# Kernel optimization log

Hardware: AMD Instinct MI355X
Metric: run time of the kernel (lower is better)

The kernel has to match this reference:

```python
import jax, jax.numpy as jnp
import numpy as np

MODEL = 2048
LATENT = 512
POS = 1024
NH = 16
HD = MODEL // NH        # 128
PHD = POS // NH         # 64
THETA = 50000.0


def _rope_tables(S, dim, base=THETA):
    inv_freq = 1.0 / (base ** (jnp.arange(0, dim, 2, dtype=jnp.float32) / dim))
    t = jnp.arange(S, dtype=jnp.float32)
    freqs = jnp.outer(t, inv_freq)                  # [S, dim/2]
    emb = jnp.concatenate([freqs, freqs], axis=-1)  # [S, dim]
    return jnp.cos(emb), jnp.sin(emb)


def _rotate_half(x):
    h = x.shape[-1] // 2
    return jnp.concatenate([-x[..., h:], x[..., :h]], axis=-1)


def _apply_rope(x, cos, sin):
    # x: [..., S, dim]; cos/sin: [S, dim]
    return x * cos + _rotate_half(x) * sin


def setup_inputs() -> dict:
    key = jax.random.key(0)
    ks = jax.random.split(key, 16)
    std = 0.02
    d = {
        'x':      jax.random.normal(ks[0], (2, 2048, MODEL), jnp.float32),
        'w_qkv':  jax.random.normal(ks[1], (MODEL, 3 * LATENT), jnp.float32) * std,
        'b_qkv':  jnp.zeros((3 * LATENT,), jnp.float32),
        'w_qup':  jax.random.normal(ks[2], (LATENT, MODEL), jnp.float32) * std,
        'b_qup':  jnp.zeros((MODEL,), jnp.float32),
        'w_kup':  jax.random.normal(ks[3], (LATENT, MODEL), jnp.float32) * std,
        'b_kup':  jnp.zeros((MODEL,), jnp.float32),
        'w_vup':  jax.random.normal(ks[4], (LATENT, MODEL), jnp.float32) * std,
        'b_vup':  jnp.zeros((MODEL,), jnp.float32),
        'w_qpos': jax.random.normal(ks[5], (LATENT, POS), jnp.float32) * std,
        'b_qpos': jnp.zeros((POS,), jnp.float32),
        'w_kpos': jax.random.normal(ks[6], (MODEL, PHD), jnp.float32) * std,
        'b_kpos': jnp.zeros((PHD,), jnp.float32),
        'w_o':    jax.random.normal(ks[7], (MODEL, MODEL), jnp.float32) * std,
        'b_o':    jnp.zeros((MODEL,), jnp.float32),
    }
    return d


def reference(x, w_qkv, b_qkv, w_qup, b_qup, w_kup, b_kup, w_vup, b_vup,
              w_qpos, b_qpos, w_kpos, b_kpos, w_o, b_o):
    B, S, _ = x.shape
    # fused down-projection into shared latent
    latent_qkv = x @ w_qkv + b_qkv                       # [B,S,3L]
    lq, lk, lv = jnp.split(latent_qkv, 3, axis=-1)       # each [B,S,L]

    cos, sin = _rope_tables(S, PHD)

    # decoupled positional key (shared across heads), RoPE on sub-slice
    pos_k = x @ w_kpos + b_kpos                          # [B,S,PHD]
    pos_k = _apply_rope(pos_k, cos, sin)

    # up-projections
    q = (lq @ w_qup + b_qup).reshape(B, S, NH, HD).transpose(0, 2, 1, 3)
    k = (lk @ w_kup + b_kup).reshape(B, S, NH, HD).transpose(0, 2, 1, 3)
    v = (lv @ w_vup + b_vup).reshape(B, S, NH, HD).transpose(0, 2, 1, 3)

    pos_q = (lq @ w_qpos + b_qpos).reshape(B, S, NH, PHD).transpose(0, 2, 1, 3)
    pos_q = _apply_rope(pos_q, cos, sin)                 # [B,NH,S,PHD]

    pos_kh = jnp.broadcast_to(pos_k[:, None], (B, NH, S, PHD))
    q = jnp.concatenate([q, pos_q], axis=-1)             # [B,NH,S,HD+PHD]
    k = jnp.concatenate([k, pos_kh], axis=-1)

    scale = 1.0 / jnp.sqrt(jnp.asarray(HD + PHD, x.dtype))
    scores = jnp.einsum('bhqd,bhkd->bhqk', q, k) * scale
    causal = jnp.tril(jnp.ones((S, S), bool))
    scores = jnp.where(causal, scores, jnp.finfo(scores.dtype).min)
    p = jax.nn.softmax(scores, axis=-1)
    attn = jnp.einsum('bhqk,bhkd->bhqd', p, v)           # [B,NH,S,HD]
    attn = attn.transpose(0, 2, 1, 3).reshape(B, S, MODEL)
    return attn @ w_o + b_o
```

## Files before the change

kernel.cpp:

```cpp
#include <hip/hip_runtime.h>
#include <cstdint>
#include <cstddef>

typedef __bf16 bf16x8 __attribute__((ext_vector_type(8)));
typedef float  f32x4  __attribute__((ext_vector_type(4)));
typedef unsigned short us8 __attribute__((ext_vector_type(8)));
typedef unsigned short us4 __attribute__((ext_vector_type(4)));

__device__ __forceinline__ unsigned short f2bf(float f) {
  union { float f; unsigned u; } v; v.f = f;
  unsigned r = v.u + 0x7FFFu + ((v.u >> 16) & 1u);
  return (unsigned short)(r >> 16);
}
__device__ __forceinline__ float b2f(unsigned short h) {
  union { unsigned u; float f; } v; v.u = ((unsigned)h) << 16;
  return v.f;
}
__device__ __forceinline__ f32x4 mfma16(bf16x8 a, bf16x8 b, f32x4 c) {
  return __builtin_amdgcn_mfma_f32_16x16x32_bf16(a, b, c, 0, 0, 0);
}
__device__ __forceinline__ void gl_lds16(const unsigned short* g, unsigned short* l) {
  __builtin_amdgcn_global_load_lds(
      (const __attribute__((address_space(1))) void*)g,
      (__attribute__((address_space(3))) void*)l, 16, 0, 0);
}

__global__ void prep_misc_kernel(const float* __restrict__ b_qkv,
                                 const float* __restrict__ b_kpos,
                                 const float* __restrict__ b_qup,
                                 const float* __restrict__ b_qpos,
                                 float* __restrict__ bias1,
                                 float* __restrict__ bias2q,
                                 float* __restrict__ costab,
                                 float* __restrict__ sintab,
                                 unsigned short* __restrict__ wB1pad) {
  int i = blockIdx.x * 256 + threadIdx.x;
  if (i < 65536) {
    int s = i >> 5, f = i & 31;
    float inv = powf(50000.0f, -(float)f / 32.0f);
    float a = (float)s * inv;
    costab[i] = cosf(a);
    sintab[i] = sinf(a);
  }
  if (i < 1664) bias1[i] = (i < 1536) ? b_qkv[i] : (i < 1600 ? b_kpos[i - 1536] : 0.0f);
  if (i < 3072) bias2q[i] = (i < 2048) ? b_qup[i] : b_qpos[i - 2048];
  if (i < 131072) wB1pad[i] = 0;
}

__global__ void convx_kernel(const float* __restrict__ in,
                             unsigned short* __restrict__ out, int n4) {
  int i = blockIdx.x * 256 + threadIdx.x;
  if (i < n4) {
    float4 v = ((const float4*)in)[i];
    us4 o;
    o[0] = f2bf(v.x); o[1] = f2bf(v.y); o[2] = f2bf(v.z); o[3] = f2bf(v.w);
    ((us4*)out)[i] = o;
  }
}

__global__ void tconv_kernel(const float* __restrict__ in, int ldin,
                             unsigned short* __restrict__ out, int ldo) {
  __shared__ float tile[32][33];
  int c0 = blockIdx.x * 32, r0 = blockIdx.y * 32;
  int tx = threadIdx.x & 31, ty = threadIdx.x >> 5;
  for (int j = 0; j < 4; ++j)
    tile[ty + j * 8][tx] = in[(size_t)(r0 + ty + j * 8) * ldin + c0 + tx];
  __syncthreads();
  for (int j = 0; j < 4; ++j)
    out[(size_t)(c0 + ty + j * 8) * ldo + r0 + tx] = f2bf(tile[tx][ty + j * 8]);
}

template <int OUT_MODE>
__global__ __launch_bounds__(256, 2)
void gemm_bt_kernel(const unsigned short* __restrict__ A, int lda,
                    const unsigned short* __restrict__ Bt, int ldb,
                    void* __restrict__ Cout, int ldc,
                    const float* __restrict__ bias, int K) {
  __shared__ unsigned short smem[OUT_MODE == 2 ? 128 * 136 : 128 * 128];
  unsigned short* Alds = smem;
  unsigned short* Blds = smem + 128 * 64;
  int tid = threadIdx.x;
  int wave = tid >> 6, lane = tid & 63;
  int g = lane >> 4, r = lane & 15;
  int wr = wave >> 1, wc = wave & 1;
  long brow = (long)blockIdx.y * 128, bcol = (long)blockIdx.x * 128;

  int srowl = lane >> 3;
  int sw = ((lane & 7) ^ (srowl & 7)) * 8;
  const unsigned short* Abase = A + (brow + wave * 32 + srowl) * (long)lda + sw;
  const unsigned short* Bbase = Bt + (bcol + wave * 32 + srowl) * (long)ldb + sw;

  f32x4 acc[4][4];
  for (int mi = 0; mi < 4; ++mi)
    for (int ni = 0; ni < 4; ++ni)
      acc[mi][ni] = f32x4{0.f, 0.f, 0.f, 0.f};

  const char* Ab = (const char*)Alds;
  const char* Bb = (const char*)Blds;
  int rx = (r & 7) << 4;

  for (int k0 = 0; k0 < K; k0 += 64) {
    for (int c = 0; c < 4; ++c) {
      gl_lds16(Abase + (size_t)c * 8 * lda + k0, Alds + (wave * 32 + c * 8) * 64);
      gl_lds16(Bbase + (size_t)c * 8 * ldb + k0, Blds + (wave * 32 + c * 8) * 64);
    }
    __syncthreads();
    for (int kk = 0; kk < 2; ++kk) {
      bf16x8 af[4], bfv[4];
      for (int mi = 0; mi < 4; ++mi)
        af[mi] = *(const bf16x8*)(Ab + (size_t)(wr * 64 + mi * 16 + r) * 128 +
                                  ((kk * 64 + g * 16) ^ rx));
      for (int ni = 0; ni < 4; ++ni)
        bfv[ni] = *(const bf16x8*)(Bb + (size_t)(wc * 64 + ni * 16 + r) * 128 +
                                   ((kk * 64 + g * 16) ^ rx));
      for (int mi = 0; mi < 4; ++mi)
        for (int ni = 0; ni < 4; ++ni)
          acc[mi][ni] = mfma16(af[mi], bfv[ni], acc[mi][ni]);
    }
    __syncthreads();
  }

  if (OUT_MODE == 2) {
    for (int mi = 0; mi < 4; ++mi)
      for (int ni = 0; ni < 4; ++ni) {
        int col = wc * 64 + ni * 16 + r;
        float bv = bias[bcol + col];
        int rowb = wr * 64 + mi * 16 + g * 4;
        for (int i = 0; i < 4; ++i)
          smem[col * 136 + rowb + i] = f2bf(acc[mi][ni][i] + bv);
      }
    __syncthreads();
    int col = tid >> 1, half = tid & 1;
    int bh = (int)(brow >> 11) * 16 + (int)(bcol >> 7);
    unsigned short* outp = (unsigned short*)Cout +
                           ((size_t)bh * 128 + col) * 2048 + (brow & 2047);
    for (int j = 0; j < 8; ++j) {
      int row0 = half * 64 + j * 8;
      *(us8*)(outp + row0) = *(const us8*)&smem[col * 136 + row0];
    }
    return;
  }

  for (int mi = 0; mi < 4; ++mi)
    for (int ni = 0; ni < 4; ++ni) {
      long col = bcol + wc * 64 + ni * 16 + r;
      float bv = bias ? bias[col] : 0.0f;
      long rowb = brow + wr * 64 + mi * 16 + g * 4;
      for (int i = 0; i < 4; ++i) {
        float v = acc[mi][ni][i] + bv;
        if (OUT_MODE == 1)
          ((float*)Cout)[(rowb + i) * (long)ldc + col] = v;
        else
          ((unsigned short*)Cout)[(rowb + i) * (long)ldc + col] = f2bf(v);
      }
    }
}

__global__ void rope_kernel(const unsigned short* __restrict__ tmp_q,
                            const unsigned short* __restrict__ latext,
                            const float* __restrict__ costab,
                            const float* __restrict__ sintab,
                            unsigned short* __restrict__ posqr,
                            unsigned short* __restrict__ poskr) {
  int idx = blockIdx.x * 256 + threadIdx.x;
  const unsigned short* src;
  unsigned short* dst;
  int s, dp0;
  if (idx < 524288) {
    int rowA = idx >> 7, rem = idx & 127;
    int h = rem >> 3;
    dp0 = (rem & 7) * 8;
    s = rowA & 2047;
    src = tmp_q + (size_t)rowA * 3072 + 2048 + h * 64;
    dst = posqr + (size_t)rowA * 1024 + h * 64 + dp0;
  } else if (idx < 557056) {
    int j = idx - 524288;
    int rowA = j >> 3;
    dp0 = (j & 7) * 8;
    s = rowA & 2047;
    src = latext + (size_t)rowA * 1664 + 1536;
    dst = poskr + (size_t)rowA * 64 + dp0;
  } else {
    return;
  }
  us8 x1 = *(const us8*)(src + dp0);
  us8 x2 = *(const us8*)(src + (dp0 ^ 32));
  int f0 = dp0 & 31;
  const float* cp = costab + s * 32 + f0;
  const float* sp = sintab + s * 32 + f0;
  bool low = dp0 < 32;
  us8 o;
  for (int e = 0; e < 8; ++e) {
    float a = b2f(x1[e]), b = b2f(x2[e]);
    float v = low ? (a * cp[e] - b * sp[e]) : (a * cp[e] + b * sp[e]);
    o[e] = f2bf(v);
  }
  *(us8*)dst = o;
}

__global__ __launch_bounds__(256, 2)
void flash_kernel(const unsigned short* __restrict__ tmp_q,
                  const unsigned short* __restrict__ tmp_k,
                  const unsigned short* __restrict__ posqr,
                  const unsigned short* __restrict__ poskr,
                  const unsigned short* __restrict__ vT,
                  unsigned short* __restrict__ ob,
                  int* __restrict__ counter) {
  const int S = 2048;
  int tid = threadIdx.x, wave = tid >> 6, lane = tid & 63;
  int g = lane >> 4, r = lane & 15;
  const float sl2 = 1.44269504f / 13.8564064605510183f;
  const float DEFER = 96.0f;

  __shared__ unsigned short Klds[32 * 192];
  __shared__ unsigned short Vlds[128 * 32];
  __shared__ unsigned short Plds[4][16][40];
  __shared__ int s_tile;
  char* Kb = (char*)Klds;
  char* Vb = (char*)Vlds;
  int rx7 = (r & 7) << 4, rx3 = (r & 3) << 4;

  for (;;) {
    if (tid == 0) s_tile = atomicAdd(counter, 1);
    __syncthreads();
    int t = s_tile;
    if (t >= 1024) return;
    int qt = 31 - (t >> 5), bh = t & 31;
    int b = bh >> 4, h = bh & 15;
    int qbase = qt * 64;
    int nchunk = 2 * (qt + 1);
    size_t rb = (size_t)b * 2048;

    const unsigned short* kpn = tmp_k + rb * 2048 + h * 128;
    const unsigned short* kpr = poskr + rb * 64;
    const unsigned short* vp = vT + (size_t)bh * 128 * S;

    bf16x8 qf[6];
    {
      size_t qrowA = rb + qbase + wave * 16 + r;
      const unsigned short* qn = tmp_q + qrowA * 3072 + h * 128 + g * 8;
      for (int c = 0; c < 4; ++c) qf[c] = *(const bf16x8*)(qn + c * 32);
      const unsigned short* qr_ = posqr + qrowA * 1024 + h * 64 + g * 8;
      qf[4] = *(const bf16x8*)(qr_);
      qf[5] = *(const bf16x8*)(qr_ + 32);
    }

    f32x4 acc[8];
    for (int d = 0; d < 8; ++d) acc[d] = f32x4{0.f, 0.f, 0.f, 0.f};
    float m_r[4], l_r[4];
    for (int i = 0; i < 4; ++i) { m_r[i] = -3.0e38f; l_r[i] = 0.f; }

    int kn_row[2], kn_seg[2];
    for (int j = 0; j < 2; ++j) {
      int slot = j * 256 + tid;
      kn_row[j] = slot >> 4;
      kn_seg[j] = slot & 15;
    }
    int kr_row = tid >> 3, kr_seg = tid & 7;
    int v_row[2], v_seg[2];
    for (int j = 0; j < 2; ++j) {
      int slot = j * 256 + tid;
      v_row[j] = slot >> 2;
      v_seg[j] = slot & 3;
    }

    us8 kreg[2], krope, vreg[2];
    for (int j = 0; j < 2; ++j)
      kreg[j] = *(const us8*)(kpn + (size_t)kn_row[j] * 2048 + kn_seg[j] * 8);
    krope = *(const us8*)(kpr + (size_t)kr_row * 64 + kr_seg * 8);
    for (int j = 0; j < 2; ++j)
      vreg[j] = *(const us8*)(vp + (size_t)v_row[j] * S + v_seg[j] * 8);

    for (int ch = 0; ch < nchunk; ++ch) {
      for (int j = 0; j < 2; ++j)
        *(us8*)(Kb + (size_t)kn_row[j] * 384 +
                ((kn_seg[j] ^ (kn_row[j] & 7)) << 4)) = kreg[j];
      *(us8*)(Kb + (size_t)kr_row * 384 +
              (((16 + kr_seg) ^ (kr_row & 7)) << 4)) = krope;
      for (int j = 0; j < 2; ++j)
        *(us8*)(Vb + (size_t)v_row[j] * 64 +
                ((v_seg[j] ^ (v_row[j] & 3)) << 4)) = vreg[j];
      __syncthreads();
      if (ch + 1 < nchunk) {
        int kv1 = (ch + 1) * 32;
        for (int j = 0; j < 2; ++j)
          kreg[j] = *(const us8*)(kpn + (size_t)(kv1 + kn_row[j]) * 2048 + kn_seg[j] * 8);
        krope = *(const us8*)(kpr + (size_t)(kv1 + kr_row) * 64 + kr_seg * 8);
        for (int j = 0; j < 2; ++j)
          vreg[j] = *(const us8*)(vp + (size_t)v_row[j] * S + kv1 + v_seg[j] * 8);
      }
      int kv0 = ch * 32;

      f32x4 sc0 = {0.f, 0.f, 0.f, 0.f}, sc1 = {0.f, 0.f, 0.f, 0.f};
      __builtin_amdgcn_s_setprio(1);
      for (int c = 0; c < 6; ++c) {
        bf16x8 kf0 = *(const bf16x8*)(Kb + (size_t)r * 384 + (((c * 4 + g) << 4) ^ rx7));
        sc0 = mfma16(qf[c], kf0, sc0);
      }
      for (int c = 0; c < 6; ++c) {
        bf16x8 kf1 = *(const bf16x8*)(Kb + (size_t)(16 + r) * 384 + (((c * 4 + g) << 4) ^ rx7));
        sc1 = mfma16(qf[c], kf1, sc1);
      }
      __builtin_amdgcn_s_setprio(0);

      int kj0 = kv0 + r, kj1 = kv0 + 16 + r;
      int qi0 = qbase + wave * 16 + g * 4;
      for (int i = 0; i < 4; ++i) {
        if (kj0 > qi0 + i) sc0[i] = -1e30f;
        if (kj1 > qi0 + i) sc1[i] = -1e30f;
      }

      float tl[4];
      bool ok = true;
      for (int i = 0; i < 4; ++i) {
        tl[i] = fmaxf(sc0[i], sc1[i]);
        ok = ok && (tl[i] - m_r[i] <= DEFER);
      }
      if (!__all(ok)) {
        for (int i = 0; i < 4; ++i) {
          float tm = tl[i];
          for (int off = 1; off < 16; off <<= 1) tm = fmaxf(tm, __shfl_xor(tm, off, 64));
          float mnew = fmaxf(m_r[i], tm);
          float corr = exp2f((m_r[i] - mnew) * sl2);
          l_r[i] *= corr;
          for (int d = 0; d < 8; ++d) acc[d][i] *= corr;
          m_r[i] = mnew;
        }
      }
      float p0[4], p1[4];
      for (int i = 0; i < 4; ++i) {
        float e0 = exp2f((sc0[i] - m_r[i]) * sl2);
        float e1 = exp2f((sc1[i] - m_r[i]) * sl2);
        float rs = e0 + e1;
        for (int off = 1; off < 16; off <<= 1) rs += __shfl_xor(rs, off, 64);
        l_r[i] += rs;
        p0[i] = e0;
        p1[i] = e1;
      }

      for (int i = 0; i < 4; ++i) {
        Plds[wave][g * 4 + i][r] = f2bf(p0[i]);
        Plds[wave][g * 4 + i][16 + r] = f2bf(p1[i]);
      }
      bf16x8 pa = *(const bf16x8*)&Plds[wave][r][g * 8];
      __builtin_amdgcn_s_setprio(1);
      for (int dt = 0; dt < 8; ++dt) {
        bf16x8 vf = *(const bf16x8*)(Vb + (size_t)(dt * 16 + r) * 64 + ((g << 4) ^ rx3));
        acc[dt] = mfma16(pa, vf, acc[dt]);
      }
      __builtin_amdgcn_s_setprio(0);
      __syncthreads();
    }

    for (int i = 0; i < 4; ++i) {
      float inv = 1.0f / l_r[i];
      int row = qbase + wave * 16 + g * 4 + i;
      size_t base = (rb + row) * 2048 + h * 128;
      for (int dt = 0; dt < 8; ++dt)
        ob[base + dt * 16 + r] = f2bf(acc[dt][i] * inv);
    }
  }
}

extern "C" void kernel_launch(void* const* d_in, const int* in_sizes, int n_in,
                              void* d_out, int out_size, void* d_ws, size_t ws_size,
                              hipStream_t stream) {
  const float* x      = (const float*)d_in[0];
  const float* w_qkv  = (const float*)d_in[1];
  const float* b_qkv  = (const float*)d_in[2];
  const float* w_qup  = (const float*)d_in[3];
  const float* b_qup  = (const float*)d_in[4];
  const float* w_kup  = (const float*)d_in[5];
  const float* b_kup  = (const float*)d_in[6];
  const float* w_vup  = (const float*)d_in[7];
  const float* b_vup  = (const float*)d_in[8];
  const float* w_qpos = (const float*)d_in[9];
  const float* b_qpos = (const float*)d_in[10];
  const float* w_kpos = (const float*)d_in[11];
  const float* b_kpos = (const float*)d_in[12];
  const float* w_o    = (const float*)d_in[13];
  const float* b_o    = (const float*)d_in[14];
  (void)in_sizes; (void)n_in; (void)out_size; (void)ws_size;

  char* ws = (char*)d_ws;
  size_t off = 0;
  auto alloc = [&](size_t bytes) -> char* {
    char* p = ws + off;
    off += (bytes + 255) & ~(size_t)255;
    return p;
  };

  unsigned short* xb     = (unsigned short*)alloc(16777216);
  unsigned short* wB1    = (unsigned short*)alloc(6815744);
  unsigned short* wB2q   = (unsigned short*)alloc(3145728);
  unsigned short* wB2k   = (unsigned short*)alloc(2097152);
  unsigned short* wB2v   = (unsigned short*)alloc(2097152);
  unsigned short* wBo    = (unsigned short*)alloc(8388608);
  float*          bias1  = (float*)alloc(1664 * 4);
  float*          bias2q = (float*)alloc(3072 * 4);
  float*          costab = (float*)alloc(262144);
  float*          sintab = (float*)alloc(262144);
  unsigned short* latext = (unsigned short*)alloc(13631488);
  unsigned short* tmp_q  = (unsigned short*)alloc(25165824);
  unsigned short* tmp_k  = (unsigned short*)alloc(16777216);
  unsigned short* vTbuf  = (unsigned short*)alloc(16777216);
  unsigned short* posqr  = (unsigned short*)alloc(8388608);
  unsigned short* poskr  = (unsigned short*)alloc(524288);
  int*            counter= (int*)alloc(256);
  unsigned short* attnb  = xb;

  prep_misc_kernel<<<512, 256, 0, stream>>>(b_qkv, b_kpos, b_qup, b_qpos,
                                            bias1, bias2q, costab, sintab,
                                            wB1 + (size_t)1600 * 2048);
  convx_kernel<<<8192, 256, 0, stream>>>(x, xb, 2097152);
  tconv_kernel<<<dim3(48, 64), 256, 0, stream>>>(w_qkv, 1536, wB1, 2048);
  tconv_kernel<<<dim3(2, 64), 256, 0, stream>>>(w_kpos, 64, wB1 + (size_t)1536 * 2048, 2048);
  tconv_kernel<<<dim3(64, 16), 256, 0, stream>>>(w_qup, 2048, wB2q, 512);
  tconv_kernel<<<dim3(32, 16), 256, 0, stream>>>(w_qpos, 1024, wB2q + (size_t)2048 * 512, 512);
  tconv_kernel<<<dim3(64, 16), 256, 0, stream>>>(w_kup, 2048, wB2k, 512);
  tconv_kernel<<<dim3(64, 16), 256, 0, stream>>>(w_vup, 2048, wB2v, 512);
  tconv_kernel<<<dim3(64, 64), 256, 0, stream>>>(w_o, 2048, wBo, 2048);

  gemm_bt_kernel<0><<<dim3(13, 32), 256, 0, stream>>>(xb, 2048, wB1, 2048,
                                                      latext, 1664, bias1, 2048);
  gemm_bt_kernel<0><<<dim3(24, 32), 256, 0, stream>>>(latext, 1664, wB2q, 512,
                                                      tmp_q, 3072, bias2q, 512);
  gemm_bt_kernel<0><<<dim3(16, 32), 256, 0, stream>>>(latext + 512, 1664, wB2k, 512,
                                                      tmp_k, 2048, b_kup, 512);
  gemm_bt_kernel<2><<<dim3(16, 32), 256, 0, stream>>>(latext + 1024, 1664, wB2v, 512,
                                                      vTbuf, 2048, b_vup, 512);
  rope_kernel<<<2176, 256, 0, stream>>>(tmp_q, latext, costab, sintab, posqr, poskr);
  hipMemsetAsync(counter, 0, 4, stream);
  flash_kernel<<<1536, 256, 0, stream>>>(tmp_q, tmp_k, posqr, poskr, vTbuf,
                                         attnb, counter);
  gemm_bt_kernel<1><<<dim3(16, 32), 256, 0, stream>>>(attnb, 2048, wBo, 2048,
                                                      d_out, 2048, b_o, 2048);
}
```

Before: 301.9 us.

## Split causal flash attention along KV into segments and merge partials

Splits each query tile's KV range into segments of up to 16 chunks, which raises the work-item count from 1024 to 2560. Heavy tiles are scheduled first to balance load across the persistent blocks. Partial unnormalized outputs (in bf16) and running max and sum statistics are written to a scratch buffer, and a new merge kernel combines them for query tiles 8 and above. This cuts the long-tail imbalance of the causal tiles, at the cost of extra global traffic, one more kernel launch, and an extra bf16 rounding of the partials.

```diff
diff --git a/kernel.cpp b/kernel.cpp
--- a/kernel.cpp
+++ b/kernel.cpp
@@ -198,6 +198,24 @@
   *(us8*)dst = o;
 }
 
+__device__ __forceinline__ void task_decode(int t, int& qt, int& seg, int& bh) {
+  if (t < 1024) {
+    qt = 31 - (t >> 7); int rem = t & 127; seg = rem >> 5; bh = rem & 31;
+  } else if (t < 1792) {
+    int t2 = t - 1024; int qi = t2 / 96; int rem = t2 - qi * 96;
+    qt = 23 - qi; seg = rem >> 5; bh = rem & 31;
+  } else if (t < 2304) {
+    int t3 = t - 1792; qt = 15 - (t3 >> 6); int rem = t3 & 63; seg = rem >> 5; bh = rem & 31;
+  } else {
+    int t4 = t - 2304; qt = 7 - (t4 >> 5); seg = 0; bh = t4 & 31;
+  }
+}
+__device__ __forceinline__ int task_slot(int qt, int seg, int bh) {
+  if (qt >= 24) return (31 - qt) * 128 + seg * 32 + bh;
+  if (qt >= 16) return 1024 + (23 - qt) * 96 + seg * 32 + bh;
+  return 1792 + (15 - qt) * 64 + seg * 32 + bh;
+}
+
 __global__ __launch_bounds__(256, 2)
 void flash_kernel(const unsigned short* __restrict__ tmp_q,
                   const unsigned short* __restrict__ tmp_k,
@@ -205,6 +223,8 @@
                   const unsigned short* __restrict__ poskr,
                   const unsigned short* __restrict__ vT,
                   unsigned short* __restrict__ ob,
+                  unsigned short* __restrict__ Opart,
+                  float* __restrict__ mlbuf,
                   int* __restrict__ counter) {
   const int S = 2048;
   int tid = threadIdx.x, wave = tid >> 6, lane = tid & 63;
@@ -220,15 +240,31 @@
   char* Vb = (char*)Vlds;
   int rx7 = (r & 7) << 4, rx3 = (r & 3) << 4;
 
+  int kn_row[2], kn_seg[2];
+  for (int j = 0; j < 2; ++j) {
+    int slot = j * 256 + tid;
+    kn_row[j] = slot >> 4;
+    kn_seg[j] = slot & 15;
+  }
+  int kr_row = tid >> 3, kr_seg = tid & 7;
+  int v_row[2], v_seg[2];
+  for (int j = 0; j < 2; ++j) {
+    int slot = j * 256 + tid;
+    v_row[j] = slot >> 2;
+    v_seg[j] = slot & 3;
+  }
+
   for (;;) {
     if (tid == 0) s_tile = atomicAdd(counter, 1);
     __syncthreads();
     int t = s_tile;
-    if (t >= 1024) return;
-    int qt = 31 - (t >> 5), bh = t & 31;
+    if (t >= 2560) return;
+    int qt, seg, bh;
+    task_decode(t, qt, seg, bh);
     int b = bh >> 4, h = bh & 15;
     int qbase = qt * 64;
-    int nchunk = 2 * (qt + 1);
+    int cbeg = seg * 16;
+    int cend = min(cbeg + 16, 2 * (qt + 1));
     size_t rb = (size_t)b * 2048;
 
     const unsigned short* kpn = tmp_k + rb * 2048 + h * 128;
@@ -250,28 +286,17 @@
     float m_r[4], l_r[4];
     for (int i = 0; i < 4; ++i) { m_r[i] = -3.0e38f; l_r[i] = 0.f; }
 
-    int kn_row[2], kn_seg[2];
-    for (int j = 0; j < 2; ++j) {
-      int slot = j * 256 + tid;
-      kn_row[j] = slot >> 4;
-      kn_seg[j] = slot & 15;
-    }
-    int kr_row = tid >> 3, kr_seg = tid & 7;
-    int v_row[2], v_seg[2];
-    for (int j = 0; j < 2; ++j) {
-      int slot = j * 256 + tid;
-      v_row[j] = slot >> 2;
-      v_seg[j] = slot & 3;
-    }
-
     us8 kreg[2], krope, vreg[2];
-    for (int j = 0; j < 2; ++j)
-      kreg[j] = *(const us8*)(kpn + (size_t)kn_row[j] * 2048 + kn_seg[j] * 8);
-    krope = *(const us8*)(kpr + (size_t)kr_row * 64 + kr_seg * 8);
-    for (int j = 0; j < 2; ++j)
-      vreg[j] = *(const us8*)(vp + (size_t)v_row[j] * S + v_seg[j] * 8);
-
-    for (int ch = 0; ch < nchunk; ++ch) {
+    {
+      int kv0 = cbeg * 32;
+      for (int j = 0; j < 2; ++j)
+        kreg[j] = *(const us8*)(kpn + (size_t)(kv0 + kn_row[j]) * 2048 + kn_seg[j] * 8);
+      krope = *(const us8*)(kpr + (size_t)(kv0 + kr_row) * 64 + kr_seg * 8);
+      for (int j = 0; j < 2; ++j)
+        vreg[j] = *(const us8*)(vp + (size_t)v_row[j] * S + kv0 + v_seg[j] * 8);
+    }
+
+    for (int ch = cbeg; ch < cend; ++ch) {
       for (int j = 0; j < 2; ++j)
         *(us8*)(Kb + (size_t)kn_row[j] * 384 +
                 ((kn_seg[j] ^ (kn_row[j] & 7)) << 4)) = kreg[j];
@@ -281,7 +306,7 @@
         *(us8*)(Vb + (size_t)v_row[j] * 64 +
                 ((v_seg[j] ^ (v_row[j] & 3)) << 4)) = vreg[j];
       __syncthreads();
-      if (ch + 1 < nchunk) {
+      if (ch + 1 < cend) {
         int kv1 = (ch + 1) * 32;
         for (int j = 0; j < 2; ++j)
           kreg[j] = *(const us8*)(kpn + (size_t)(kv1 + kn_row[j]) * 2048 + kn_seg[j] * 8);
@@ -352,13 +377,77 @@
       __syncthreads();
     }
 
-    for (int i = 0; i < 4; ++i) {
-      float inv = 1.0f / l_r[i];
-      int row = qbase + wave * 16 + g * 4 + i;
-      size_t base = (rb + row) * 2048 + h * 128;
-      for (int dt = 0; dt < 8; ++dt)
-        ob[base + dt * 16 + r] = f2bf(acc[dt][i] * inv);
-    }
+    if (qt <= 7) {
+      for (int i = 0; i < 4; ++i) {
+        float inv = 1.0f / l_r[i];
+        int row = qbase + wave * 16 + g * 4 + i;
+        size_t base = (rb + row) * 2048 + h * 128;
+        for (int dt = 0; dt < 8; ++dt)
+          ob[base + dt * 16 + r] = f2bf(acc[dt][i] * inv);
+      }
+    } else {
+      unsigned short* op = Opart + (size_t)t * 8192;
+      for (int i = 0; i < 4; ++i) {
+        int row = wave * 16 + g * 4 + i;
+        for (int dt = 0; dt < 8; ++dt)
+          op[row * 128 + dt * 16 + r] = f2bf(acc[dt][i]);
+        if (r == 0) {
+          mlbuf[(size_t)t * 128 + row * 2]     = m_r[i];
+          mlbuf[(size_t)t * 128 + row * 2 + 1] = l_r[i];
+        }
+      }
+    }
+  }
+}
+
+__global__ void merge_kernel(const unsigned short* __restrict__ Opart,
+                             const float* __restrict__ mlbuf,
+                             unsigned short* __restrict__ ob) {
+  int qt = 8 + (blockIdx.x >> 5), bh = blockIdx.x & 31;
+  int b = bh >> 4, h = bh & 15;
+  int tid = threadIdx.x;
+  int row = tid >> 2, c0 = (tid & 3) * 32;
+  const float sl2 = 1.44269504f / 13.8564064605510183f;
+  int ns = (qt >= 24) ? 4 : (qt >= 16 ? 3 : 2);
+
+  size_t slot[4];
+  float m[4], l[4], w[4];
+  float M = -3.0e38f;
+#pragma unroll
+  for (int j = 0; j < 4; ++j) {
+    if (j < ns) {
+      slot[j] = task_slot(qt, j, bh);
+      m[j] = mlbuf[slot[j] * 128 + row * 2];
+      l[j] = mlbuf[slot[j] * 128 + row * 2 + 1];
+      M = fmaxf(M, m[j]);
+    }
+  }
+  float L = 0.f;
+#pragma unroll
+  for (int j = 0; j < 4; ++j)
+    if (j < ns) { w[j] = exp2f((m[j] - M) * sl2); L += w[j] * l[j]; }
+  float invL = 1.f / L;
+#pragma unroll
+  for (int j = 0; j < 4; ++j) if (j < ns) w[j] *= invL;
+
+  float o[32];
+#pragma unroll
+  for (int e = 0; e < 32; ++e) o[e] = 0.f;
+#pragma unroll
+  for (int j = 0; j < 4; ++j) {
+    if (j < ns) {
+      const unsigned short* pp = Opart + slot[j] * 8192 + row * 128 + c0;
+      for (int blk = 0; blk < 4; ++blk) {
+        us8 v = *(const us8*)(pp + blk * 8);
+        for (int e = 0; e < 8; ++e) o[blk * 8 + e] += w[j] * b2f(v[e]);
+      }
+    }
+  }
+  size_t obase = ((size_t)b * 2048 + qt * 64 + row) * 2048 + h * 128 + c0;
+  for (int blk = 0; blk < 4; ++blk) {
+    us8 st;
+    for (int e = 0; e < 8; ++e) st[e] = f2bf(o[blk * 8 + e]);
+    *(us8*)(ob + obase + blk * 8) = st;
   }
 }
 
@@ -406,6 +495,8 @@
   unsigned short* vTbuf  = (unsigned short*)alloc(16777216);
   unsigned short* posqr  = (unsigned short*)alloc(8388608);
   unsigned short* poskr  = (unsigned short*)alloc(524288);
+  unsigned short* Opart  = (unsigned short*)alloc(41943040);
+  float*          mlbuf  = (float*)alloc(1310720);
   int*            counter= (int*)alloc(256);
   unsigned short* attnb  = xb;
 
@@ -432,7 +523,8 @@
   rope_kernel<<<2176, 256, 0, stream>>>(tmp_q, latext, costab, sintab, posqr, poskr);
   hipMemsetAsync(counter, 0, 4, stream);
   flash_kernel<<<1536, 256, 0, stream>>>(tmp_q, tmp_k, posqr, poskr, vTbuf,
-                                         attnb, counter);
+                                         attnb, Opart, mlbuf, counter);
+  merge_kernel<<<768, 256, 0, stream>>>(Opart, mlbuf, attnb);
   gemm_bt_kernel<1><<<dim3(16, 32), 256, 0, stream>>>(attnb, 2048, wBo, 2048,
                                                       d_out, 2048, b_o, 2048);
 }
```

Result: slower. 338.5 us (+12.1%).
